# Kernel optimization log

Measured on AMD Instinct MI355X. Metric: run time of the kernel, lower is better.

Reference implementation:

```python
import jax, jax.numpy as jnp
import numpy as np
import math

CHUNK = 128


def setup_inputs() -> dict:
    key = jax.random.key(0)
    ks = jax.random.split(key, 12)
    B, S, H, D = 2, 4096, 1024, 2048  # D = hidden_dim * expansion_factor
    std = 0.02
    inp = {
        "hidden_states": jax.random.normal(ks[0], (B, S, H), jnp.float32),
        "Wq": jax.random.normal(ks[1], (H, D), jnp.float32) * std,
        "bq": jnp.zeros((D,), jnp.float32),
        "Wk": jax.random.normal(ks[2], (H, D), jnp.float32) * std,
        "bk": jnp.zeros((D,), jnp.float32),
        "Wv": jax.random.normal(ks[3], (H, D), jnp.float32) * std,
        "bv": jnp.zeros((D,), jnp.float32),
        "Wg": jax.random.normal(ks[4], (H, D), jnp.float32) * std,
        "bg": jnp.zeros((D,), jnp.float32),
        "Wo": jax.random.normal(ks[5], (D, H), jnp.float32) * std,
        "bo": jnp.zeros((H,), jnp.float32),
    }
    return inp


def reference(hidden_states, Wq, bq, Wk, bk, Wv, bv, Wg, bg, Wo, bo):
    B, S, H = hidden_states.shape
    D = Wq.shape[1]
    cs = CHUNK
    nC = S // cs  # seq_len chosen as multiple of chunk_size (no padding path)

    q = hidden_states @ Wq + bq
    k = hidden_states @ Wk + bk
    v = hidden_states @ Wv + bv
    gate = jax.nn.sigmoid(hidden_states @ Wg + bg)

    qc = q.reshape(B, nC, cs, D)
    kc = k.reshape(B, nC, cs, D)
    vc = v.reshape(B, nC, cs, D)
    gc = gate.reshape(B, nC, cs, D)

    # intra-chunk causal softmax attention (vectorized over all chunks)
    scale = 1.0 / math.sqrt(D)
    attn = jnp.einsum('bncd,bnkd->bnck', qc, kc) * scale  # [B,nC,cs,cs]
    causal = jnp.tril(jnp.ones((cs, cs), bool))
    attn = jnp.where(causal, attn, -jnp.inf)
    attn = jax.nn.softmax(attn, axis=-1)
    local = jnp.einsum('bnck,bnkd->bncd', attn, vc)

    # inter-chunk linear-attention state accumulation:
    # cross_i = q_i @ sum_{j<i} K_j^T V_j  (sequential scan over chunks)
    def step(state, xs):
        qi, ki, vi = xs  # each [B,cs,D]
        cross = jnp.einsum('bcd,bde->bce', qi, state)
        state = state + jnp.einsum('bcd,bce->bde', ki, vi)
        return state, cross

    state0 = jnp.zeros((B, D, D), hidden_states.dtype)
    _, cross = jax.lax.scan(
        step, state0,
        (qc.transpose(1, 0, 2, 3), kc.transpose(1, 0, 2, 3), vc.transpose(1, 0, 2, 3)))
    cross = cross.transpose(1, 0, 2, 3)  # [B,nC,cs,D]

    out = (local + cross) * gc
    out = out.reshape(B, S, D)
    return out @ Wo + bo
```

## Files before the change

kernel.cpp:

```cpp
#include <hip/hip_runtime.h>
#include <hip/hip_bf16.h>
#include <math.h>


typedef __bf16 bf16_t;
typedef __bf16 bf16x8 __attribute__((ext_vector_type(8)));
typedef __bf16 bf16x4 __attribute__((ext_vector_type(4)));
typedef float f32x4 __attribute__((ext_vector_type(4)));

#define NB_ 2
#define SEQ 4096
#define HID 1024
#define DD 2048
#define BS 8192
#define LDS_TB 73728

__device__ __forceinline__ void async16(const void* g, void* l) {
  __builtin_amdgcn_global_load_lds(
      (const __attribute__((address_space(1))) void*)g,
      (__attribute__((address_space(3))) void*)l, 16, 0, 0);
}

#define VMW0 asm volatile("s_waitcnt vmcnt(0)" ::: "memory")
#define BARR __builtin_amdgcn_s_barrier()
#define FEN asm volatile("" ::: "memory")

template <int WM, int WN>
__device__ __forceinline__ void coreTB(const bf16_t* __restrict__ A, int lda,
                                       const bf16_t* __restrict__ B, int ldb, int nt,
                                       bf16_t* lds, f32x4 (&acc)[4][4]) {
  constexpr int T = WM * WN * 64;
  constexpr int AE = WM * 64 * 32;
  constexpr int BUF = AE + WN * 64 * 32;
  constexpr int NISS = BUF / (T * 8);
  const int t = threadIdx.x;
  const int lane = t & 63, w = t >> 6;
  const int wm = w / WN, wn = w % WN;
  const int lr = lane & 15, lg = lane >> 4;

  int aOff[4], bOff[4];
#pragma unroll
  for (int f = 0; f < 4; ++f) {
    int ra = wm * 64 + f * 16 + lr;
    aOff[f] = ra * 32 + (((lg + (ra >> 1)) & 3) << 3);
    int rb = wn * 64 + f * 16 + lr;
    bOff[f] = AE + rb * 32 + (((lg + (rb >> 1)) & 3) << 3);
  }
  int src[NISS];
#pragma unroll
  for (int q = 0; q < NISS; ++q) {
    int e = q * T * 8 + t * 8;
    bool isB = (q * T * 8) >= AE;
    int e2 = isB ? e - AE : e;
    int r = e2 >> 5;
    int g = (((e2 >> 3) & 3) - (r >> 1)) & 3;
    src[q] = r * (isB ? ldb : lda) + g * 8;
  }
#pragma unroll
  for (int m = 0; m < 4; ++m)
#pragma unroll
    for (int n = 0; n < 4; ++n) acc[m][n] = (f32x4){0.f, 0.f, 0.f, 0.f};

#pragma unroll
  for (int q = 0; q < NISS; ++q) {
    bool isB = (q * T * 8) >= AE;
    async16((isB ? B : A) + src[q], lds + q * T * 8 + t * 8);
  }
  {
    const int k1 = (1 < nt ? 1 : 0) << 5;
#pragma unroll
    for (int q = 0; q < NISS; ++q) {
      bool isB = (q * T * 8) >= AE;
      async16((isB ? B : A) + k1 + src[q], lds + BUF + q * T * 8 + t * 8);
    }
  }

  for (int tt = 0; tt < nt; ++tt) {
    bf16_t* cur = lds + (tt % 3) * BUF;
    bf16_t* nxt = lds + ((tt + 2) % 3) * BUF;
    const int kn = (tt + 2 < nt ? tt + 2 : 0) << 5;
    if constexpr (NISS == 3) {
      asm volatile("s_waitcnt vmcnt(3)" ::: "memory");
    } else if constexpr (NISS == 4) {
      asm volatile("s_waitcnt vmcnt(4)" ::: "memory");
    } else {
      asm volatile("s_waitcnt vmcnt(0)" ::: "memory");
    }
    BARR; FEN;
    bf16x8 af[4], bv[4];
#pragma unroll
    for (int f = 0; f < 4; ++f) af[f] = *reinterpret_cast<const bf16x8*>(&cur[aOff[f]]);
#pragma unroll
    for (int f = 0; f < 4; ++f) bv[f] = *reinterpret_cast<const bf16x8*>(&cur[bOff[f]]);
#pragma unroll
    for (int q = 0; q < NISS; ++q) {
      bool isB = (q * T * 8) >= AE;
      async16((isB ? B : A) + kn + src[q], nxt + q * T * 8 + t * 8);
    }
    __builtin_amdgcn_s_setprio(1);
#pragma unroll
    for (int mf = 0; mf < 4; ++mf)
#pragma unroll
      for (int nf = 0; nf < 4; ++nf)
        acc[mf][nf] =
            __builtin_amdgcn_mfma_f32_16x16x32_bf16(af[mf], bv[nf], acc[mf][nf], 0, 0, 0);
    __builtin_amdgcn_s_setprio(0);
  }
  VMW0;
  BARR; FEN;
}

__global__ void k_prep(const float* __restrict__ hs, const float* __restrict__ W0,
                       const float* __restrict__ W1, const float* __restrict__ W2,
                       const float* __restrict__ W3, const float* __restrict__ Wo,
                       bf16_t* __restrict__ hsb, bf16_t* __restrict__ Wt4,
                       bf16_t* __restrict__ Wot) {
  int z = blockIdx.z;
  int t = threadIdx.x;
  if (z == 5) {
    const float4* in4 = (const float4*)hs;
    bf16x4* out4 = (bf16x4*)hsb;
    int base = (blockIdx.y * 32 + blockIdx.x) * 256 + t;
#pragma unroll
    for (int j = 0; j < 8; ++j) {
      int i = base + j * 262144;
      float4 v = in4[i];
      bf16x4 o;
      o[0] = (bf16_t)v.x; o[1] = (bf16_t)v.y; o[2] = (bf16_t)v.z; o[3] = (bf16_t)v.w;
      out4[i] = o;
    }
    return;
  }
  __shared__ bf16_t tile[64][65];
  int c = t & 63, r0 = t >> 6;
  if (z < 4) {
    if (blockIdx.y >= 16) return;
    const float* in = z == 0 ? W0 : z == 1 ? W1 : z == 2 ? W2 : W3;
    bf16_t* o = Wt4 + (long)z * DD * HID;
    int bc = blockIdx.x, br = blockIdx.y;
#pragma unroll
    for (int rr = 0; rr < 64; rr += 4) {
      int r = rr + r0;
      tile[r][c] = (bf16_t)in[(long)(br * 64 + r) * DD + bc * 64 + c];
    }
    __syncthreads();
#pragma unroll
    for (int rr = 0; rr < 64; rr += 4) {
      int r = rr + r0;
      o[(long)(bc * 64 + r) * HID + br * 64 + c] = tile[c][r];
    }
  } else {
    if (blockIdx.x >= 16) return;
    int bc = blockIdx.x, br = blockIdx.y;
#pragma unroll
    for (int rr = 0; rr < 64; rr += 4) {
      int r = rr + r0;
      tile[r][c] = (bf16_t)Wo[(long)(br * 64 + r) * HID + bc * 64 + c];
    }
    __syncthreads();
#pragma unroll
    for (int rr = 0; rr < 64; rr += 4) {
      int r = rr + r0;
      Wot[(long)(bc * 64 + r) * DD + br * 64 + c] = tile[c][r];
    }
  }
}

__global__ __launch_bounds__(512, 4) void k_gemm_qkvg(
    const bf16_t* __restrict__ hsb, const bf16_t* __restrict__ Wt4,
    const float* __restrict__ bq, const float* __restrict__ bk,
    const float* __restrict__ bv, const float* __restrict__ bg,
    bf16_t* __restrict__ out, bf16_t* __restrict__ Vt) {
  extern __shared__ bf16_t lds[];
  const int SP = 136;
  const int SPT = 264;
  int i = blockIdx.x;
  int xcd = i & 7, g = i >> 3;
  int mb = g >> 3;
  int nb = xcd * 8 + (g & 7);
  f32x4 acc[4][4];
  coreTB<4, 2>(hsb + (long)mb * 256 * HID, HID, Wt4 + (long)nb * 128 * HID, HID,
               HID / 32, lds, acc);
  const int t = threadIdx.x, lane = t & 63, w = t >> 6;
  const int wm = w >> 1, wn = w & 1, lr = lane & 15, lg = lane >> 4;
  int z = nb >> 4;
  const float* bias = z == 0 ? bq : z == 1 ? bk : z == 2 ? bv : bg;
  int colT = (nb & 15) * 128;
  float b4[4];
#pragma unroll
  for (int nf = 0; nf < 4; ++nf) b4[nf] = bias[colT + wn * 64 + nf * 16 + lr];
  if (z != 2) {
#pragma unroll
    for (int mf = 0; mf < 4; ++mf)
#pragma unroll
      for (int reg = 0; reg < 4; ++reg) {
        int lrow = wm * 64 + mf * 16 + lg * 4 + reg;
#pragma unroll
        for (int nf = 0; nf < 4; ++nf) {
          float v = acc[mf][nf][reg] + b4[nf];
          if (z == 3) v = 1.f / (1.f + __expf(-v));
          lds[lrow * SP + wn * 64 + nf * 16 + lr] = (bf16_t)v;
        }
      }
    __syncthreads();
    bf16_t* O = out + (long)z * BS * DD + (long)mb * 256 * DD + colT;
#pragma unroll
    for (int it = 0; it < 8; ++it) {
      int s = it * 512 + t;
      int row = s >> 4, sg = s & 15;
      bf16x8 v = *reinterpret_cast<const bf16x8*>(&lds[row * SP + sg * 8]);
      *reinterpret_cast<bf16x8*>(&O[(long)row * DD + sg * 8]) = v;
    }
  } else {
#pragma unroll
    for (int mf = 0; mf < 4; ++mf)
#pragma unroll
      for (int reg = 0; reg < 4; ++reg) {
        int lrow = wm * 64 + mf * 16 + lg * 4 + reg;
#pragma unroll
        for (int nf = 0; nf < 4; ++nf) {
          int d = wn * 64 + nf * 16 + lr;
          lds[d * SPT + lrow] = (bf16_t)(acc[mf][nf][reg] + b4[nf]);
        }
      }
    __syncthreads();
    int bz = mb >> 4, smb = mb & 15;
    bf16_t* Vd = Vt + ((long)bz * DD + colT) * SEQ + smb * 256;
#pragma unroll
    for (int it = 0; it < 8; ++it) {
      int s = it * 512 + t;
      int d = s >> 5, sg = s & 31;
      bf16x8 v = *reinterpret_cast<const bf16x8*>(&lds[d * SPT + sg * 8]);
      *reinterpret_cast<bf16x8*>(&Vd[(long)d * SEQ + sg * 8]) = v;
    }
  }
}

__global__ __launch_bounds__(512, 4) void k_pair(const bf16_t* __restrict__ Q,
                                                 const bf16_t* __restrict__ Kb,
                                                 bf16_t* __restrict__ P) {
  extern __shared__ bf16_t lds[];
  int p = blockIdx.x, b = blockIdx.y;
  int c = 0, base = 0;
  while (base + (c >> 1) + 1 <= p) { base += (c >> 1) + 1; ++c; }
  int jt = p - base;
  f32x4 acc[4][4];
  coreTB<2, 4>(Q + ((long)b * SEQ + (long)c * 128) * DD, DD,
               Kb + ((long)b * SEQ + (long)jt * 256) * DD, DD, DD / 32, lds, acc);
  const int t = threadIdx.x, lane = t & 63, w = t >> 6;
  const int wm = w >> 2, wn = w & 3, lr = lane & 15, lg = lane >> 4;
  bf16_t* Pt = P + ((long)b * SEQ + (long)c * 128) * (long)SEQ + (long)jt * 256;
  const bool hasDiag = (jt == (c >> 1));
  const int side = c & 1;
  const float scale = 0.02209708691207961f;
  float* smf = (float*)lds;
#pragma unroll
  for (int mf = 0; mf < 4; ++mf)
#pragma unroll
    for (int reg = 0; reg < 4; ++reg) {
      int row = wm * 64 + mf * 16 + lg * 4 + reg;
#pragma unroll
      for (int nf = 0; nf < 4; ++nf) {
        int col = wn * 64 + nf * 16 + lr;
        float v = acc[mf][nf][reg];
        if (hasDiag && ((col >> 7) == side)) {
          int cc = col & 127;
          float sv = v * scale;
          smf[row * 128 + ((cc + row) & 127)] = (cc <= row) ? sv : -1e30f;
        } else {
          if (hasDiag && side == 0 && (col >> 7) == 1) v = 0.f;
          Pt[(long)row * SEQ + col] = (bf16_t)v;
        }
      }
    }
  if (hasDiag) {
    __syncthreads();
    if (t < 128) {
      int r = t;
      float mx = -1e30f;
      for (int cc = 0; cc <= r; ++cc) mx = fmaxf(mx, smf[r * 128 + ((cc + r) & 127)]);
      float s = 0.f;
      for (int cc = 0; cc <= r; ++cc) s += __expf(smf[r * 128 + ((cc + r) & 127)] - mx);
      float inv = 1.f / s;
      for (int cc = 0; cc < 128; ++cc) {
        float v = (cc <= r) ? __expf(smf[r * 128 + ((cc + r) & 127)] - mx) * inv : 0.f;
        Pt[(long)r * SEQ + side * 128 + cc] = (bf16_t)v;
      }
    }
  }
}

__global__ __launch_bounds__(512, 4) void k_gemm2(const bf16_t* __restrict__ P,
                                                  const bf16_t* __restrict__ Vt,
                                                  const bf16_t* __restrict__ G,
                                                  bf16_t* __restrict__ OutPre) {
  extern __shared__ bf16_t lds[];
  int bid = blockIdx.x;
  int nb = bid & 7;
  int tmp = bid >> 3;
  int mq = 31 - (tmp >> 1);
  int b = tmp & 1;
  f32x4 acc[4][4];
  coreTB<2, 4>(P + ((long)b * SEQ + (long)mq * 128) * (long)SEQ, SEQ,
               Vt + (long)b * DD * SEQ + (long)nb * 256 * SEQ, SEQ, (mq + 1) * 4,
               lds, acc);
  const int t = threadIdx.x, lane = t & 63, w = t >> 6;
  const int wm = w >> 2, wn = w & 3, lr = lane & 15, lg = lane >> 4;
#pragma unroll
  for (int mf = 0; mf < 4; ++mf)
#pragma unroll
    for (int reg = 0; reg < 4; ++reg) {
      long row = (long)b * SEQ + (long)mq * 128 + wm * 64 + mf * 16 + lg * 4 + reg;
#pragma unroll
      for (int nf = 0; nf < 4; ++nf) {
        long idx = row * DD + nb * 256 + wn * 64 + nf * 16 + lr;
        float g = (float)G[idx];
        OutPre[idx] = (bf16_t)(acc[mf][nf][reg] * g);
      }
    }
}

__global__ __launch_bounds__(512, 4) void k_gemm3(const bf16_t* __restrict__ OutPre,
                                                  const bf16_t* __restrict__ Wot,
                                                  const float* __restrict__ bo,
                                                  float* __restrict__ out) {
  extern __shared__ bf16_t lds[];
  int mb = blockIdx.x >> 2, nb = blockIdx.x & 3;
  f32x4 acc[4][4];
  coreTB<2, 4>(OutPre + (long)mb * 128 * DD, DD, Wot + (long)nb * 256 * DD, DD,
               DD / 32, lds, acc);
  const int t = threadIdx.x, lane = t & 63, w = t >> 6;
  const int wm = w >> 2, wn = w & 3, lr = lane & 15, lg = lane >> 4;
  int colbase = nb * 256 + wn * 64;
  float b4[4];
#pragma unroll
  for (int nf = 0; nf < 4; ++nf) b4[nf] = bo[colbase + nf * 16 + lr];
#pragma unroll
  for (int mf = 0; mf < 4; ++mf)
#pragma unroll
    for (int reg = 0; reg < 4; ++reg) {
      long row = mb * 128 + wm * 64 + mf * 16 + lg * 4 + reg;
#pragma unroll
      for (int nf = 0; nf < 4; ++nf)
        out[row * HID + colbase + nf * 16 + lr] = acc[mf][nf][reg] + b4[nf];
    }
}

extern "C" void kernel_launch(void* const* d_in, const int* in_sizes, int n_in,
                              void* d_out, int out_size, void* d_ws, size_t ws_size,
                              hipStream_t stream) {
  const float* hs = (const float*)d_in[0];
  const float* Wq = (const float*)d_in[1];
  const float* bq = (const float*)d_in[2];
  const float* Wk = (const float*)d_in[3];
  const float* bk = (const float*)d_in[4];
  const float* Wv = (const float*)d_in[5];
  const float* bv = (const float*)d_in[6];
  const float* Wg = (const float*)d_in[7];
  const float* bg = (const float*)d_in[8];
  const float* Wo = (const float*)d_in[9];
  const float* bo = (const float*)d_in[10];
  float* out = (float*)d_out;

  char* ws = (char*)d_ws;
  const size_t MB = 1024 * 1024;
  bf16_t* P = (bf16_t*)(ws);
  bf16_t* hsb = (bf16_t*)(ws);
  bf16_t* Wt4 = (bf16_t*)(ws + 16 * MB);
  bf16_t* Wot = (bf16_t*)(ws + 64 * MB);
  bf16_t* QKVG = (bf16_t*)(ws + 68 * MB);
  bf16_t* Vt = (bf16_t*)(ws + 196 * MB);

  bf16_t* Qb = QKVG;
  bf16_t* Kbuf = QKVG + (long)BS * DD;
  bf16_t* Vbuf = QKVG + 2l * BS * DD;
  bf16_t* Gbuf = QKVG + 3l * BS * DD;
  bf16_t* OutPre = Vbuf;

  hipFuncSetAttribute((const void*)k_gemm_qkvg,
                      hipFuncAttributeMaxDynamicSharedMemorySize, LDS_TB);
  hipFuncSetAttribute((const void*)k_pair,
                      hipFuncAttributeMaxDynamicSharedMemorySize, LDS_TB);
  hipFuncSetAttribute((const void*)k_gemm2,
                      hipFuncAttributeMaxDynamicSharedMemorySize, LDS_TB);
  hipFuncSetAttribute((const void*)k_gemm3,
                      hipFuncAttributeMaxDynamicSharedMemorySize, LDS_TB);

  k_prep<<<dim3(32, 32, 6), 256, 0, stream>>>(hs, Wq, Wk, Wv, Wg, Wo, hsb, Wt4, Wot);

  k_gemm_qkvg<<<2048, 512, LDS_TB, stream>>>(hsb, Wt4, bq, bk, bv, bg, QKVG, Vt);

  k_pair<<<dim3(272, 2), 512, LDS_TB, stream>>>(Qb, Kbuf, P);

  k_gemm2<<<512, 512, LDS_TB, stream>>>(P, Vt, Gbuf, OutPre);

  k_gemm3<<<256, 512, LDS_TB, stream>>>(OutPre, Wot, bo, out);
}
```

Measured before the change: 428.0 us.

## Load B operand directly to registers and triple-buffer A in QKVG GEMM

Adds a new GEMM core for the QKVG projection that streams only the A tile (hidden states) into LDS through a 3-stage async ring. Each wave reads its B (weight) fragments straight from global memory into registers, double-buffered across k-steps. The aim is to cut LDS traffic and capacity for the B operand and overlap global loads with MFMA work, while keeping a single barrier per k-step. The cost is more VGPR pressure and uncoalesced per-wave global reads of B, which is duplicated across the four wm waves that share each wn. The LDS size passed at launch is lowered, although 3 stages of 8192 elements use only about 48KB of it.

```diff
diff --git a/kernel.cpp b/kernel.cpp
--- a/kernel.cpp
+++ b/kernel.cpp
@@ -14,6 +14,7 @@
 #define DD 2048
 #define BS 8192
 #define LDS_TB 73728
+#define LDS_HB 69632
 
 __device__ __forceinline__ void async16(const void* g, void* l) {
   __builtin_amdgcn_global_load_lds(
@@ -21,6 +22,7 @@
       (__attribute__((address_space(3))) void*)l, 16, 0, 0);
 }
 
+#define VMW(n) asm volatile("s_waitcnt vmcnt(" #n ")" ::: "memory")
 #define VMW0 asm volatile("s_waitcnt vmcnt(0)" ::: "memory")
 #define BARR __builtin_amdgcn_s_barrier()
 #define FEN asm volatile("" ::: "memory")
@@ -105,6 +107,104 @@
         acc[mf][nf] =
             __builtin_amdgcn_mfma_f32_16x16x32_bf16(af[mf], bv[nf], acc[mf][nf], 0, 0, 0);
     __builtin_amdgcn_s_setprio(0);
+  }
+  VMW0;
+  BARR; FEN;
+}
+
+__device__ __forceinline__ void coreHB(const bf16_t* __restrict__ A, int lda,
+                                       const bf16_t* __restrict__ B, int ldb, int nt,
+                                       bf16_t* lds, f32x4 (&acc)[4][4]) {
+  const int t = threadIdx.x, lane = t & 63, w = t >> 6;
+  const int wm = w >> 1, wn = w & 1;
+  const int lr = lane & 15, lg = lane >> 4;
+  int aOff[4];
+#pragma unroll
+  for (int f = 0; f < 4; ++f) {
+    int ra = wm * 64 + f * 16 + lr;
+    aOff[f] = ra * 32 + (((lg + (ra >> 1)) & 3) << 3);
+  }
+  int srcA[2];
+#pragma unroll
+  for (int q = 0; q < 2; ++q) {
+    int e = q * 4096 + t * 8;
+    int r = e >> 5;
+    int g = (((e >> 3) & 3) - (r >> 1)) & 3;
+    srcA[q] = r * lda + g * 8;
+  }
+  const bf16_t* bp = B + (long)(wn * 64 + lr) * ldb + lg * 8;
+#pragma unroll
+  for (int m = 0; m < 4; ++m)
+#pragma unroll
+    for (int n = 0; n < 4; ++n) acc[m][n] = (f32x4){0.f, 0.f, 0.f, 0.f};
+
+  async16(A + srcA[0], lds + t * 8);
+  async16(A + srcA[1], lds + 4096 + t * 8);
+  FEN;
+  bf16x8 bvA0, bvA1, bvA2, bvA3, bvB0, bvB1, bvB2, bvB3;
+  bvA0 = *reinterpret_cast<const bf16x8*>(bp + 0l * 16 * ldb);
+  bvA1 = *reinterpret_cast<const bf16x8*>(bp + 1l * 16 * ldb);
+  bvA2 = *reinterpret_cast<const bf16x8*>(bp + 2l * 16 * ldb);
+  bvA3 = *reinterpret_cast<const bf16x8*>(bp + 3l * 16 * ldb);
+  FEN;
+  {
+    const int k1 = (1 < nt ? 1 : 0) << 5;
+    async16(A + k1 + srcA[0], lds + 8192 + t * 8);
+    async16(A + k1 + srcA[1], lds + 8192 + 4096 + t * 8);
+  }
+  FEN;
+
+  for (int tt = 0; tt < nt; tt += 2) {
+    VMW(2); BARR; FEN;
+    {
+      bf16_t* cur = lds + (tt % 3) * 8192;
+      const int kB = ((tt + 1 < nt ? tt + 1 : 0) << 5);
+      bvB0 = *reinterpret_cast<const bf16x8*>(bp + 0l * 16 * ldb + kB);
+      bvB1 = *reinterpret_cast<const bf16x8*>(bp + 1l * 16 * ldb + kB);
+      bvB2 = *reinterpret_cast<const bf16x8*>(bp + 2l * 16 * ldb + kB);
+      bvB3 = *reinterpret_cast<const bf16x8*>(bp + 3l * 16 * ldb + kB);
+      FEN;
+      const int kA = ((tt + 2 < nt ? tt + 2 : 0) << 5);
+      bf16_t* nA = lds + ((tt + 2) % 3) * 8192;
+      async16(A + kA + srcA[0], nA + t * 8);
+      async16(A + kA + srcA[1], nA + 4096 + t * 8);
+      FEN;
+      __builtin_amdgcn_s_setprio(1);
+#pragma unroll
+      for (int mf = 0; mf < 4; ++mf) {
+        bf16x8 af = *reinterpret_cast<const bf16x8*>(&cur[aOff[mf]]);
+        acc[mf][0] = __builtin_amdgcn_mfma_f32_16x16x32_bf16(af, bvA0, acc[mf][0], 0, 0, 0);
+        acc[mf][1] = __builtin_amdgcn_mfma_f32_16x16x32_bf16(af, bvA1, acc[mf][1], 0, 0, 0);
+        acc[mf][2] = __builtin_amdgcn_mfma_f32_16x16x32_bf16(af, bvA2, acc[mf][2], 0, 0, 0);
+        acc[mf][3] = __builtin_amdgcn_mfma_f32_16x16x32_bf16(af, bvA3, acc[mf][3], 0, 0, 0);
+      }
+      __builtin_amdgcn_s_setprio(0);
+    }
+    VMW(2); BARR; FEN;
+    {
+      bf16_t* cur = lds + ((tt + 1) % 3) * 8192;
+      const int kB = ((tt + 2 < nt ? tt + 2 : 0) << 5);
+      bvA0 = *reinterpret_cast<const bf16x8*>(bp + 0l * 16 * ldb + kB);
+      bvA1 = *reinterpret_cast<const bf16x8*>(bp + 1l * 16 * ldb + kB);
+      bvA2 = *reinterpret_cast<const bf16x8*>(bp + 2l * 16 * ldb + kB);
+      bvA3 = *reinterpret_cast<const bf16x8*>(bp + 3l * 16 * ldb + kB);
+      FEN;
+      const int kA = ((tt + 3 < nt ? tt + 3 : 0) << 5);
+      bf16_t* nA = lds + ((tt + 3) % 3) * 8192;
+      async16(A + kA + srcA[0], nA + t * 8);
+      async16(A + kA + srcA[1], nA + 4096 + t * 8);
+      FEN;
+      __builtin_amdgcn_s_setprio(1);
+#pragma unroll
+      for (int mf = 0; mf < 4; ++mf) {
+        bf16x8 af = *reinterpret_cast<const bf16x8*>(&cur[aOff[mf]]);
+        acc[mf][0] = __builtin_amdgcn_mfma_f32_16x16x32_bf16(af, bvB0, acc[mf][0], 0, 0, 0);
+        acc[mf][1] = __builtin_amdgcn_mfma_f32_16x16x32_bf16(af, bvB1, acc[mf][1], 0, 0, 0);
+        acc[mf][2] = __builtin_amdgcn_mfma_f32_16x16x32_bf16(af, bvB2, acc[mf][2], 0, 0, 0);
+        acc[mf][3] = __builtin_amdgcn_mfma_f32_16x16x32_bf16(af, bvB3, acc[mf][3], 0, 0, 0);
+      }
+      __builtin_amdgcn_s_setprio(0);
+    }
   }
   VMW0;
   BARR; FEN;
@@ -179,8 +279,8 @@
   int mb = g >> 3;
   int nb = xcd * 8 + (g & 7);
   f32x4 acc[4][4];
-  coreTB<4, 2>(hsb + (long)mb * 256 * HID, HID, Wt4 + (long)nb * 128 * HID, HID,
-               HID / 32, lds, acc);
+  coreHB(hsb + (long)mb * 256 * HID, HID, Wt4 + (long)nb * 128 * HID, HID,
+         HID / 32, lds, acc);
   const int t = threadIdx.x, lane = t & 63, w = t >> 6;
   const int wm = w >> 1, wn = w & 1, lr = lane & 15, lg = lane >> 4;
   int z = nb >> 4;
@@ -378,7 +478,7 @@
   bf16_t* OutPre = Vbuf;
 
   hipFuncSetAttribute((const void*)k_gemm_qkvg,
-                      hipFuncAttributeMaxDynamicSharedMemorySize, LDS_TB);
+                      hipFuncAttributeMaxDynamicSharedMemorySize, LDS_HB);
   hipFuncSetAttribute((const void*)k_pair,
                       hipFuncAttributeMaxDynamicSharedMemorySize, LDS_TB);
   hipFuncSetAttribute((const void*)k_gemm2,
@@ -388,7 +488,7 @@
 
   k_prep<<<dim3(32, 32, 6), 256, 0, stream>>>(hs, Wq, Wk, Wv, Wg, Wo, hsb, Wt4, Wot);
 
-  k_gemm_qkvg<<<2048, 512, LDS_TB, stream>>>(hsb, Wt4, bq, bk, bv, bg, QKVG, Vt);
+  k_gemm_qkvg<<<2048, 512, LDS_HB, stream>>>(hsb, Wt4, bq, bk, bv, bg, QKVG, Vt);
 
   k_pair<<<dim3(272, 2), 512, LDS_TB, stream>>>(Qb, Kbuf, P);
 
```

After: 559.2 us. 1.31x slower.
